# Performance work log

Measured on AMD Instinct MI355X. Metric: run time of the kernel, lower is better.

## Reference

```python
import jax, jax.numpy as jnp
import numpy as np

N, E, IN_DIM, OUT_DIM, EDGE_DIM = 50000, 800000, 256, 128, 64
NEG_SLOPE = 0.2


def setup_inputs() -> dict:
    key = jax.random.key(0)
    ks = jax.random.split(key, 8)
    xavier = lambda k, shape: jax.random.normal(k, shape, jnp.float32) * np.float32(np.sqrt(2.0 / (shape[0] + shape[1])))
    return {
        "nfeat": jax.random.normal(ks[0], (N, IN_DIM), jnp.float32),
        "ex": jax.random.normal(ks[1], (E, EDGE_DIM), jnp.float32),
        "src": jax.random.randint(ks[2], (E,), 0, N),
        "dst": jax.random.randint(ks[3], (E,), 0, N),
        "W_fc": xavier(ks[4], (OUT_DIM, IN_DIM)),
        "b_fc": jnp.zeros((OUT_DIM,), jnp.float32),
        "W_att": xavier(ks[5], (1, 2 * OUT_DIM + EDGE_DIM)),
        "b_att": jnp.zeros((1,), jnp.float32),
        "W_edge": xavier(ks[6], (OUT_DIM, EDGE_DIM)),
        "b_edge": jnp.zeros((OUT_DIM,), jnp.float32),
        "W_eatt": xavier(ks[7], (EDGE_DIM, EDGE_DIM)),
        "b_eatt": jnp.zeros((EDGE_DIM,), jnp.float32),
    }


def reference(nfeat, ex, src, dst, W_fc, b_fc, W_att, b_att, W_edge, b_edge, W_eatt, b_eatt):
    n = nfeat.shape[0]
    # node transform: z = fc(nfeat)  [N, OUT]
    z = nfeat @ W_fc.T + b_fc
    # edge transform for attention score calc  [E, EDGE_DIM]
    ex_t = ex @ W_eatt.T + b_eatt
    z_src = z[src]                                   # [E, OUT] gather
    # attention logits on concat[z_src, z_dst, ex_t]  [E, 1]
    z2 = jnp.concatenate([z_src, z[dst], ex_t], axis=1)
    e = jax.nn.leaky_relu(z2 @ W_att.T + b_att, NEG_SLOPE)
    # edge feature message  [E, OUT]
    ez = ex @ W_edge.T + b_edge
    # segment softmax over incoming edges of each dst node
    m = jax.ops.segment_max(e, dst, num_segments=n)  # [N, 1]
    w = jnp.exp(e - m[dst])
    denom = jax.ops.segment_sum(w, dst, num_segments=n)
    alpha = w / denom[dst]                           # [E, 1]
    # h = sum_e alpha * z_src + sum_e alpha * ez (apply_attention_on_edge)
    h = jax.ops.segment_sum(alpha * (z_src + ez), dst, num_segments=n)  # [N, OUT]
    return h, alpha
```

## Files before the change

### kernel.cpp

```cpp
#include <hip/hip_runtime.h>
#include <math.h>
#include <float.h>

#define IN_D 256
#define OUT_D 128
#define ED_D 64
#define NEG 0.2f

typedef __attribute__((ext_vector_type(8))) short bf16x8;
typedef __attribute__((ext_vector_type(4))) float f32x4;

__device__ __forceinline__ unsigned short f2bf(float f) {
    unsigned u = __float_as_uint(f);
    unsigned r = (u + 0x7FFFu + ((u >> 16) & 1u)) >> 16;
    return (unsigned short)r;
}
__device__ __forceinline__ float bf2f(unsigned short h) {
    return __uint_as_float((unsigned)h << 16);
}

__global__ __launch_bounds__(256) void k_init(
        const float* __restrict__ W_att, const float* __restrict__ b_att,
        const float* __restrict__ W_eatt, const float* __restrict__ b_eatt,
        const float* __restrict__ W_fc, const float* __restrict__ W_edge,
        float* __restrict__ u, float* __restrict__ c0,
        unsigned short* __restrict__ Wb, float2* __restrict__ Wt2,
        int* __restrict__ cnt, int N) {
    int idx = blockIdx.x * 256 + threadIdx.x;
    if (idx < N) cnt[idx] = 0;
    if (idx < IN_D * OUT_D) {
        int i = idx & 7;
        int lane = (idx >> 3) & 63;
        int rest = idx >> 9;
        int nt = rest & 7, ks = rest >> 3;
        int col = nt * 16 + (lane & 15);
        int k = ks * 32 + (lane >> 4) * 8 + i;
        Wb[idx] = f2bf(W_fc[col * IN_D + k]);
    }
    if (idx < ED_D * (OUT_D / 2)) {
        int k = idx >> 6, l = idx & 63;
        Wt2[idx] = make_float2(W_edge[(2 * l) * ED_D + k], W_edge[(2 * l + 1) * ED_D + k]);
    }
    if (idx < ED_D) {
        float acc = 0.f;
        for (int j = 0; j < ED_D; ++j) acc += W_att[256 + j] * W_eatt[j * ED_D + idx];
        u[idx] = acc;
    }
    if (idx == ED_D) {
        float c = 0.f;
        for (int j = 0; j < ED_D; ++j) c += W_att[256 + j] * b_eatt[j];
        c0[0] = c + b_att[0];
    }
}

__global__ __launch_bounds__(256) void k_hist(const int* __restrict__ dst,
                                              int* __restrict__ cnt,
                                              int* __restrict__ rank, int E) {
    int i = blockIdx.x * 256 + threadIdx.x;
    if (i < E) rank[i] = atomicAdd(&cnt[dst[i]], 1);
}

#define LDA 272
__global__ __launch_bounds__(256) void k_node(
        const float* __restrict__ nfeat, const unsigned short* __restrict__ Wb,
        const float* __restrict__ b_fc, const float* __restrict__ W_att,
        unsigned short* __restrict__ zb, float* __restrict__ asrc,
        float* __restrict__ adst, int n) {
    __shared__ unsigned short sa[128 * LDA];
    int t = threadIdx.x;
    int row_base = blockIdx.x * 128;

    int r8 = t >> 3, c8 = t & 7;
#pragma unroll
    for (int p = 0; p < 4; ++p) {
        int r = p * 32 + r8;
        int node = row_base + r; if (node >= n) node = n - 1;
        const float4* srcp = (const float4*)(nfeat + (size_t)node * IN_D);
#pragma unroll
        for (int q = 0; q < 8; ++q) {
            int c4 = q * 8 + c8;
            float4 v = srcp[c4];
            unsigned pk0 = (unsigned)f2bf(v.x) | ((unsigned)f2bf(v.y) << 16);
            unsigned pk1 = (unsigned)f2bf(v.z) | ((unsigned)f2bf(v.w) << 16);
            *(uint2*)&sa[(size_t)r * LDA + c4 * 4] = make_uint2(pk0, pk1);
        }
    }
    __syncthreads();

    int lane = t & 63, w = t >> 6;
    int lr = lane & 15, lg = lane >> 4;

    f32x4 acc[2][8];
#pragma unroll
    for (int mi = 0; mi < 2; ++mi)
#pragma unroll
        for (int nt = 0; nt < 8; ++nt) acc[mi][nt] = (f32x4)(0.f);

    const bf16x8* wb8 = (const bf16x8*)Wb;
#pragma unroll
    for (int ks = 0; ks < 8; ++ks) {
        bf16x8 af[2], bfr[8];
#pragma unroll
        for (int mi = 0; mi < 2; ++mi) {
            int row = (2 * w + mi) * 16 + lr;
            af[mi] = *(const bf16x8*)&sa[(size_t)row * LDA + ks * 32 + lg * 8];
        }
#pragma unroll
        for (int nt = 0; nt < 8; ++nt)
            bfr[nt] = wb8[(ks * 8 + nt) * 64 + lane];
#pragma unroll
        for (int mi = 0; mi < 2; ++mi)
#pragma unroll
            for (int nt = 0; nt < 8; ++nt)
                acc[mi][nt] = __builtin_amdgcn_mfma_f32_16x16x32_bf16(
                    af[mi], bfr[nt], acc[mi][nt], 0, 0, 0);
    }

    float w1c[8], w2c[8], bfc[8];
#pragma unroll
    for (int nt = 0; nt < 8; ++nt) {
        int col = nt * 16 + lr;
        w1c[nt] = W_att[col];
        w2c[nt] = W_att[128 + col];
        bfc[nt] = b_fc[col];
    }
#pragma unroll
    for (int mi = 0; mi < 2; ++mi) {
        float p1[4] = {0.f, 0.f, 0.f, 0.f}, p2[4] = {0.f, 0.f, 0.f, 0.f};
#pragma unroll
        for (int nt = 0; nt < 8; ++nt) {
#pragma unroll
            for (int reg = 0; reg < 4; ++reg) {
                float zv = acc[mi][nt][reg] + bfc[nt];
                int m = row_base + (2 * w + mi) * 16 + lg * 4 + reg;
                if (m < n) zb[(size_t)m * OUT_D + nt * 16 + lr] = f2bf(zv);
                p1[reg] = fmaf(zv, w1c[nt], p1[reg]);
                p2[reg] = fmaf(zv, w2c[nt], p2[reg]);
            }
        }
#pragma unroll
        for (int reg = 0; reg < 4; ++reg) {
#pragma unroll
            for (int off = 1; off <= 8; off <<= 1) {
                p1[reg] += __shfl_xor(p1[reg], off);
                p2[reg] += __shfl_xor(p2[reg], off);
            }
        }
        if (lr == 0) {
#pragma unroll
            for (int reg = 0; reg < 4; ++reg) {
                int m = row_base + (2 * w + mi) * 16 + lg * 4 + reg;
                if (m < n) { asrc[m] = p1[reg]; adst[m] = p2[reg]; }
            }
        }
    }
}

__global__ __launch_bounds__(1024) void k_scan(const int* __restrict__ cnt,
                                               int* __restrict__ rowptr, int N) {
    int t = threadIdx.x;
    int per = (N + 1023) / 1024;
    int b0 = t * per, b1 = b0 + per;
    if (b0 > N) b0 = N;
    if (b1 > N) b1 = N;
    int s = 0;
    for (int i = b0; i < b1; ++i) s += cnt[i];
    int wl = t & 63, w = t >> 6;
    int v = s;
#pragma unroll
    for (int off = 1; off < 64; off <<= 1) {
        int a = __shfl_up(v, off);
        if (wl >= off) v += a;
    }
    __shared__ int wsum[16], woff[16];
    if (wl == 63) wsum[w] = v;
    __syncthreads();
    if (t == 0) { int r = 0; for (int i = 0; i < 16; ++i) { woff[i] = r; r += wsum[i]; } }
    __syncthreads();
    int run = woff[w] + v - s;
    for (int i = b0; i < b1; ++i) { rowptr[i] = run; run += cnt[i]; }
    if (t == 1023) rowptr[N] = run;
}

__global__ __launch_bounds__(256) void k_fill(
        const int* __restrict__ dst, const int* __restrict__ src,
        const int* __restrict__ rank, const int* __restrict__ rowptr,
        int* __restrict__ eid_csr, int* __restrict__ src_csr, int E) {
    int i = blockIdx.x * 256 + threadIdx.x;
    if (i >= E) return;
    int d = dst[i];
    int pos = rowptr[d] + rank[i];
    eid_csr[pos] = i;
    src_csr[pos] = src[i];
}

__global__ __launch_bounds__(256) void k_fused(
        const unsigned short* __restrict__ zb, const float* __restrict__ ex,
        const int* __restrict__ eid_csr, const int* __restrict__ src_csr,
        const int* __restrict__ rowptr,
        const float* __restrict__ asrc, const float* __restrict__ adst,
        const float* __restrict__ u, const float* __restrict__ c0,
        float* __restrict__ h, float* __restrict__ alpha_out,
        float* __restrict__ xsum, int N) {
    int lane = threadIdx.x & 63;
    int half = lane >> 5, hl = lane & 31;
    int n = blockIdx.x * 4 + (threadIdx.x >> 6);
    if (n >= N) return;
    int beg = rowptr[n], end = rowptr[n + 1];
    int deg = end - beg;
    if (deg == 0) return;
    float adn = adst[n], cc = c0[0];
    const float2* ex2 = (const float2*)ex;
    const ushort4* z4 = (const ushort4*)zb;

    if (deg <= 64) {
        int el = 0, sl = 0;
        if (lane < deg) {
            el = eid_csr[beg + lane];
            sl = src_csr[beg + lane];
        }
        int qh = lane >> 4, ql = lane & 15;
        const float4* ex4 = (const float4*)ex;
        float4 u4q = ((const float4*)u)[ql];
        float lg = -FLT_MAX;
        for (int j = 0; j < deg; j += 4) {
            int jq = j + qh;
            int eq = __shfl(el, (jq < deg) ? jq : (deg - 1));
            float4 xv = ex4[(size_t)eq * 16 + ql];
            float d = fmaf(xv.x, u4q.x, fmaf(xv.y, u4q.y, fmaf(xv.z, u4q.z, xv.w * u4q.w)));
            d += __shfl_xor(d, 8);
            d += __shfl_xor(d, 4);
            d += __shfl_xor(d, 2);
            d += __shfl_xor(d, 1);
            int rel = lane - j;
            float dl = __shfl(d, (rel & 3) * 16);
            if (rel >= 0 && rel < 4 && lane < deg) lg = dl;
        }
        if (lane < deg) {
            lg += asrc[sl] + adn + cc;
            lg = (lg > 0.f) ? lg : NEG * lg;
        }
        float m = lg;
#pragma unroll
        for (int off = 32; off >= 1; off >>= 1) m = fmaxf(m, __shfl_xor(m, off));
        float wvv = (lane < deg) ? expf(lg - m) : 0.f;
        float sw = wvv;
#pragma unroll
        for (int off = 32; off >= 1; off >>= 1) sw += __shfl_xor(sw, off);
        float al = wvv / sw;
        if (lane < deg) alpha_out[el] = al;
        float4 accz = make_float4(0.f, 0.f, 0.f, 0.f);
        float2 accx = make_float2(0.f, 0.f);
        int j = 0;
        for (; j + 8 <= deg; j += 8) {
            float a[4]; int s[4], e[4];
#pragma unroll
            for (int q = 0; q < 4; ++q) {
                int idx = j + 2 * q + half;
                a[q] = __shfl(al, idx);
                s[q] = __shfl(sl, idx);
                e[q] = __shfl(el, idx);
            }
            ushort4 zu[4]; float2 xv[4];
#pragma unroll
            for (int q = 0; q < 4; ++q) {
                zu[q] = z4[(size_t)s[q] * 32 + hl];
                xv[q] = ex2[(size_t)e[q] * 32 + hl];
            }
#pragma unroll
            for (int q = 0; q < 4; ++q) {
                accz.x = fmaf(a[q], bf2f(zu[q].x), accz.x);
                accz.y = fmaf(a[q], bf2f(zu[q].y), accz.y);
                accz.z = fmaf(a[q], bf2f(zu[q].z), accz.z);
                accz.w = fmaf(a[q], bf2f(zu[q].w), accz.w);
                accx.x = fmaf(a[q], xv[q].x, accx.x);
                accx.y = fmaf(a[q], xv[q].y, accx.y);
            }
        }
        if (j + 4 <= deg) {
            float a[2]; int s[2], e[2];
#pragma unroll
            for (int q = 0; q < 2; ++q) {
                int idx = j + 2 * q + half;
                a[q] = __shfl(al, idx);
                s[q] = __shfl(sl, idx);
                e[q] = __shfl(el, idx);
            }
            ushort4 zu[2]; float2 xv[2];
#pragma unroll
            for (int q = 0; q < 2; ++q) {
                zu[q] = z4[(size_t)s[q] * 32 + hl];
                xv[q] = ex2[(size_t)e[q] * 32 + hl];
            }
#pragma unroll
            for (int q = 0; q < 2; ++q) {
                accz.x = fmaf(a[q], bf2f(zu[q].x), accz.x);
                accz.y = fmaf(a[q], bf2f(zu[q].y), accz.y);
                accz.z = fmaf(a[q], bf2f(zu[q].z), accz.z);
                accz.w = fmaf(a[q], bf2f(zu[q].w), accz.w);
                accx.x = fmaf(a[q], xv[q].x, accx.x);
                accx.y = fmaf(a[q], xv[q].y, accx.y);
            }
            j += 4;
        }
        for (; j < deg; j += 2) {
            int idx = j + half;
            float a = __shfl(al, idx);
            int s = __shfl(sl, idx), e = __shfl(el, idx);
            ushort4 zu = z4[(size_t)s * 32 + hl];
            float2 xv = ex2[(size_t)e * 32 + hl];
            accz.x = fmaf(a, bf2f(zu.x), accz.x);
            accz.y = fmaf(a, bf2f(zu.y), accz.y);
            accz.z = fmaf(a, bf2f(zu.z), accz.z);
            accz.w = fmaf(a, bf2f(zu.w), accz.w);
            accx.x = fmaf(a, xv.x, accx.x);
            accx.y = fmaf(a, xv.y, accx.y);
        }
        accz.x += __shfl_xor(accz.x, 32);
        accz.y += __shfl_xor(accz.y, 32);
        accz.z += __shfl_xor(accz.z, 32);
        accz.w += __shfl_xor(accz.w, 32);
        accx.x += __shfl_xor(accx.x, 32);
        accx.y += __shfl_xor(accx.y, 32);
        if (half == 0) {
            ((float4*)h)[(size_t)n * 32 + hl] = accz;
            ((float2*)xsum)[(size_t)n * 32 + hl] = accx;
        }
    } else {
        float uv = u[lane];
        float m = -FLT_MAX, ssum = 0.f;
        for (int i = beg; i < end; ++i) {
            int e = eid_csr[i];
            float xv = ex[(size_t)e * ED_D + lane];
            float p = xv * uv;
#pragma unroll
            for (int off = 32; off >= 1; off >>= 1) p += __shfl_xor(p, off);
            float lg = p + asrc[src_csr[i]] + adn + cc;
            lg = (lg > 0.f) ? lg : NEG * lg;
            float mn = fmaxf(m, lg);
            ssum = ssum * expf(m - mn) + expf(lg - mn);
            m = mn;
        }
        float rden = 1.f / ssum;
        const ushort2* z2 = (const ushort2*)zb;
        float2 accz2 = make_float2(0.f, 0.f);
        float accxs = 0.f;
        for (int i = beg; i < end; ++i) {
            int e = eid_csr[i];
            int s = src_csr[i];
            float xv = ex[(size_t)e * ED_D + lane];
            float p = xv * uv;
#pragma unroll
            for (int off = 32; off >= 1; off >>= 1) p += __shfl_xor(p, off);
            float lg = p + asrc[s] + adn + cc;
            lg = (lg > 0.f) ? lg : NEG * lg;
            float al = expf(lg - m) * rden;
            if (lane == 0) alpha_out[e] = al;
            accxs = fmaf(al, xv, accxs);
            ushort2 zz = z2[(size_t)s * ED_D + lane];
            accz2.x = fmaf(al, bf2f(zz.x), accz2.x);
            accz2.y = fmaf(al, bf2f(zz.y), accz2.y);
        }
        ((float2*)h)[(size_t)n * ED_D + lane] = accz2;
        xsum[(size_t)n * ED_D + lane] = accxs;
    }
}

__global__ __launch_bounds__(256) void k_xmm(
        const float2* __restrict__ Wt2, const float* __restrict__ b_edge,
        const float* __restrict__ xsum, const int* __restrict__ rowptr,
        float2* __restrict__ h2, int N) {
    __shared__ float2 swt[ED_D * 64];
    for (int i = threadIdx.x; i < ED_D * 64; i += 256) swt[i] = Wt2[i];
    __syncthreads();
    int lane = threadIdx.x & 63;
    int wv = threadIdx.x >> 6;
    float2 be2 = ((const float2*)b_edge)[lane];
    for (int n = blockIdx.x * 4 + wv; n < N; n += gridDim.x * 4) {
        int deg = rowptr[n + 1] - rowptr[n];
        if (deg == 0) {
            h2[(size_t)n * 64 + lane] = make_float2(0.f, 0.f);
            continue;
        }
        float xk = xsum[(size_t)n * 64 + lane];
        float2 hv = h2[(size_t)n * 64 + lane];
        hv.x += be2.x; hv.y += be2.y;
#pragma unroll 8
        for (int k = 0; k < 64; ++k) {
            float a = __shfl(xk, k);
            float2 w2 = swt[k * 64 + lane];
            hv.x = fmaf(a, w2.x, hv.x);
            hv.y = fmaf(a, w2.y, hv.y);
        }
        h2[(size_t)n * 64 + lane] = hv;
    }
}

extern "C" void kernel_launch(void* const* d_in, const int* in_sizes, int n_in,
                              void* d_out, int out_size, void* d_ws, size_t ws_size,
                              hipStream_t stream) {
    const float* nfeat = (const float*)d_in[0];
    const float* ex    = (const float*)d_in[1];
    const int*   src   = (const int*)d_in[2];
    const int*   dst   = (const int*)d_in[3];
    const float* W_fc  = (const float*)d_in[4];
    const float* b_fc  = (const float*)d_in[5];
    const float* W_att = (const float*)d_in[6];
    const float* b_att = (const float*)d_in[7];
    const float* W_edge = (const float*)d_in[8];
    const float* b_edge = (const float*)d_in[9];
    const float* W_eatt = (const float*)d_in[10];
    const float* b_eatt = (const float*)d_in[11];
    int N = in_sizes[0] / IN_D;
    int E = in_sizes[2];

    float* h_out = (float*)d_out;
    float* alpha_out = h_out + (size_t)N * OUT_D;

    char* w = (char*)d_ws;
    auto alloc = [&](size_t bytes) { char* p = w; w += (bytes + 255) & ~255ull; return p; };
    unsigned short* zb = (unsigned short*)alloc((size_t)N * OUT_D * 2);
    float* asrc   = (float*)alloc((size_t)N * 4);
    float* adst   = (float*)alloc((size_t)N * 4);
    int* cnt      = (int*)alloc((size_t)N * 4);
    int* rowptr   = (int*)alloc(((size_t)N + 1) * 4);
    int* rank     = (int*)alloc((size_t)E * 4);
    int* eid_csr  = (int*)alloc((size_t)E * 4);
    int* src_csr  = (int*)alloc((size_t)E * 4);
    float* xsum   = (float*)alloc((size_t)N * ED_D * 4);
    unsigned short* Wb = (unsigned short*)alloc((size_t)IN_D * OUT_D * 2);
    float2* Wt2   = (float2*)alloc((size_t)ED_D * 64 * 8);
    float* u      = (float*)alloc(64 * 4);
    float* c0     = (float*)alloc(4);

    int init_total = N > IN_D * OUT_D ? N : IN_D * OUT_D;
    k_init<<<(init_total + 255) / 256, 256, 0, stream>>>(
        W_att, b_att, W_eatt, b_eatt, W_fc, W_edge, u, c0, Wb, Wt2, cnt, N);
    k_hist<<<(E + 255) / 256, 256, 0, stream>>>(dst, cnt, rank, E);
    k_node<<<(N + 127) / 128, 256, 0, stream>>>(nfeat, Wb, b_fc, W_att, zb, asrc, adst, N);
    k_scan<<<1, 1024, 0, stream>>>(cnt, rowptr, N);
    k_fill<<<(E + 255) / 256, 256, 0, stream>>>(dst, src, rank, rowptr, eid_csr, src_csr, E);
    k_fused<<<(N + 3) / 4, 256, 0, stream>>>(zb, ex, eid_csr, src_csr, rowptr, asrc, adst,
                                             u, c0, h_out, alpha_out, xsum, N);
    k_xmm<<<(N + 3) / 4, 256, 0, stream>>>((const float2*)Wt2, b_edge, xsum, rowptr,
                                           (float2*)h_out, N);
}
```

Measured before the change: 349.0 us.

## Assign one half-wave per destination node and pack CSR indices as int2

The fused aggregation kernel now assigns 32 lanes per destination node, eight nodes per block, instead of a full 64-lane wavefront per node. Average degree is about 16, so the wider mapping left many lanes idle. The cross-half reduction is gone, and the high-degree path now uses vectorised float2/ushort4 loads over 32 lanes. Edge id and source id are also packed into one int2 CSR array, so each edge needs one load instead of two. The risks are serialised gathers per edge within a half-wave and a lower degree threshold for the slower online-softmax path.

Result: slower. 380.9 us (+9.1%).

```diff
diff --git a/kernel.cpp b/kernel.cpp
--- a/kernel.cpp
+++ b/kernel.cpp
@@ -185,81 +185,81 @@
 __global__ __launch_bounds__(256) void k_fill(
         const int* __restrict__ dst, const int* __restrict__ src,
         const int* __restrict__ rank, const int* __restrict__ rowptr,
-        int* __restrict__ eid_csr, int* __restrict__ src_csr, int E) {
+        int2* __restrict__ csr2, int E) {
     int i = blockIdx.x * 256 + threadIdx.x;
     if (i >= E) return;
     int d = dst[i];
     int pos = rowptr[d] + rank[i];
-    eid_csr[pos] = i;
-    src_csr[pos] = src[i];
+    csr2[pos] = make_int2(i, src[i]);
 }
 
 __global__ __launch_bounds__(256) void k_fused(
         const unsigned short* __restrict__ zb, const float* __restrict__ ex,
-        const int* __restrict__ eid_csr, const int* __restrict__ src_csr,
-        const int* __restrict__ rowptr,
+        const int2* __restrict__ csr2, const int* __restrict__ rowptr,
         const float* __restrict__ asrc, const float* __restrict__ adst,
         const float* __restrict__ u, const float* __restrict__ c0,
         float* __restrict__ h, float* __restrict__ alpha_out,
         float* __restrict__ xsum, int N) {
-    int lane = threadIdx.x & 63;
-    int half = lane >> 5, hl = lane & 31;
-    int n = blockIdx.x * 4 + (threadIdx.x >> 6);
+    int hl = threadIdx.x & 31;
+    int hb = (threadIdx.x & 63) & 32;
+    int n = blockIdx.x * 8 + (threadIdx.x >> 5);
     if (n >= N) return;
     int beg = rowptr[n], end = rowptr[n + 1];
     int deg = end - beg;
     if (deg == 0) return;
     float adn = adst[n], cc = c0[0];
     const float2* ex2 = (const float2*)ex;
+    const float4* ex4 = (const float4*)ex;
     const ushort4* z4 = (const ushort4*)zb;
 
-    if (deg <= 64) {
+    if (deg <= 32) {
         int el = 0, sl = 0;
-        if (lane < deg) {
-            el = eid_csr[beg + lane];
-            sl = src_csr[beg + lane];
-        }
-        int qh = lane >> 4, ql = lane & 15;
-        const float4* ex4 = (const float4*)ex;
+        if (hl < deg) { int2 r = csr2[beg + hl]; el = r.x; sl = r.y; }
+        int qq = hl >> 4, ql = hl & 15;
         float4 u4q = ((const float4*)u)[ql];
         float lg = -FLT_MAX;
-        for (int j = 0; j < deg; j += 4) {
-            int jq = j + qh;
-            int eq = __shfl(el, (jq < deg) ? jq : (deg - 1));
+        for (int j = 0; j < deg; j += 2) {
+            int jq = j + qq;
+            int eq = __shfl(el, hb + ((jq < deg) ? jq : (deg - 1)));
             float4 xv = ex4[(size_t)eq * 16 + ql];
             float d = fmaf(xv.x, u4q.x, fmaf(xv.y, u4q.y, fmaf(xv.z, u4q.z, xv.w * u4q.w)));
             d += __shfl_xor(d, 8);
             d += __shfl_xor(d, 4);
             d += __shfl_xor(d, 2);
             d += __shfl_xor(d, 1);
-            int rel = lane - j;
-            float dl = __shfl(d, (rel & 3) * 16);
-            if (rel >= 0 && rel < 4 && lane < deg) lg = dl;
-        }
-        if (lane < deg) {
+            int rel = hl - j;
+            float dl = __shfl(d, hb + (rel & 1) * 16);
+            if (rel >= 0 && rel < 2 && hl < deg) lg = dl;
+        }
+        if (hl < deg) {
             lg += asrc[sl] + adn + cc;
             lg = (lg > 0.f) ? lg : NEG * lg;
         }
         float m = lg;
-#pragma unroll
-        for (int off = 32; off >= 1; off >>= 1) m = fmaxf(m, __shfl_xor(m, off));
-        float wvv = (lane < deg) ? expf(lg - m) : 0.f;
+        m = fmaxf(m, __shfl_xor(m, 16));
+        m = fmaxf(m, __shfl_xor(m, 8));
+        m = fmaxf(m, __shfl_xor(m, 4));
+        m = fmaxf(m, __shfl_xor(m, 2));
+        m = fmaxf(m, __shfl_xor(m, 1));
+        float wvv = (hl < deg) ? expf(lg - m) : 0.f;
         float sw = wvv;
-#pragma unroll
-        for (int off = 32; off >= 1; off >>= 1) sw += __shfl_xor(sw, off);
+        sw += __shfl_xor(sw, 16);
+        sw += __shfl_xor(sw, 8);
+        sw += __shfl_xor(sw, 4);
+        sw += __shfl_xor(sw, 2);
+        sw += __shfl_xor(sw, 1);
         float al = wvv / sw;
-        if (lane < deg) alpha_out[el] = al;
+        if (hl < deg) alpha_out[el] = al;
         float4 accz = make_float4(0.f, 0.f, 0.f, 0.f);
         float2 accx = make_float2(0.f, 0.f);
         int j = 0;
-        for (; j + 8 <= deg; j += 8) {
+        for (; j + 4 <= deg; j += 4) {
             float a[4]; int s[4], e[4];
 #pragma unroll
             for (int q = 0; q < 4; ++q) {
-                int idx = j + 2 * q + half;
-                a[q] = __shfl(al, idx);
-                s[q] = __shfl(sl, idx);
-                e[q] = __shfl(el, idx);
+                a[q] = __shfl(al, hb + j + q);
+                s[q] = __shfl(sl, hb + j + q);
+                e[q] = __shfl(el, hb + j + q);
             }
             ushort4 zu[4]; float2 xv[4];
 #pragma unroll
@@ -277,36 +277,9 @@
                 accx.y = fmaf(a[q], xv[q].y, accx.y);
             }
         }
-        if (j + 4 <= deg) {
-            float a[2]; int s[2], e[2];
-#pragma unroll
-            for (int q = 0; q < 2; ++q) {
-                int idx = j + 2 * q + half;
-                a[q] = __shfl(al, idx);
-                s[q] = __shfl(sl, idx);
-                e[q] = __shfl(el, idx);
-            }
-            ushort4 zu[2]; float2 xv[2];
-#pragma unroll
-            for (int q = 0; q < 2; ++q) {
-                zu[q] = z4[(size_t)s[q] * 32 + hl];
-                xv[q] = ex2[(size_t)e[q] * 32 + hl];
-            }
-#pragma unroll
-            for (int q = 0; q < 2; ++q) {
-                accz.x = fmaf(a[q], bf2f(zu[q].x), accz.x);
-                accz.y = fmaf(a[q], bf2f(zu[q].y), accz.y);
-                accz.z = fmaf(a[q], bf2f(zu[q].z), accz.z);
-                accz.w = fmaf(a[q], bf2f(zu[q].w), accz.w);
-                accx.x = fmaf(a[q], xv[q].x, accx.x);
-                accx.y = fmaf(a[q], xv[q].y, accx.y);
-            }
-            j += 4;
-        }
-        for (; j < deg; j += 2) {
-            int idx = j + half;
-            float a = __shfl(al, idx);
-            int s = __shfl(sl, idx), e = __shfl(el, idx);
+        for (; j < deg; ++j) {
+            float a = __shfl(al, hb + j);
+            int s = __shfl(sl, hb + j), e = __shfl(el, hb + j);
             ushort4 zu = z4[(size_t)s * 32 + hl];
             float2 xv = ex2[(size_t)e * 32 + hl];
             accz.x = fmaf(a, bf2f(zu.x), accz.x);
@@ -316,53 +289,52 @@
             accx.x = fmaf(a, xv.x, accx.x);
             accx.y = fmaf(a, xv.y, accx.y);
         }
-        accz.x += __shfl_xor(accz.x, 32);
-        accz.y += __shfl_xor(accz.y, 32);
-        accz.z += __shfl_xor(accz.z, 32);
-        accz.w += __shfl_xor(accz.w, 32);
-        accx.x += __shfl_xor(accx.x, 32);
-        accx.y += __shfl_xor(accx.y, 32);
-        if (half == 0) {
-            ((float4*)h)[(size_t)n * 32 + hl] = accz;
-            ((float2*)xsum)[(size_t)n * 32 + hl] = accx;
-        }
+        ((float4*)h)[(size_t)n * 32 + hl] = accz;
+        ((float2*)xsum)[(size_t)n * 32 + hl] = accx;
     } else {
-        float uv = u[lane];
+        float2 u2 = ((const float2*)u)[hl];
         float m = -FLT_MAX, ssum = 0.f;
         for (int i = beg; i < end; ++i) {
-            int e = eid_csr[i];
-            float xv = ex[(size_t)e * ED_D + lane];
-            float p = xv * uv;
-#pragma unroll
-            for (int off = 32; off >= 1; off >>= 1) p += __shfl_xor(p, off);
-            float lg = p + asrc[src_csr[i]] + adn + cc;
-            lg = (lg > 0.f) ? lg : NEG * lg;
-            float mn = fmaxf(m, lg);
-            ssum = ssum * expf(m - mn) + expf(lg - mn);
+            int2 r = csr2[i];
+            float2 xv = ex2[(size_t)r.x * 32 + hl];
+            float p = fmaf(xv.x, u2.x, xv.y * u2.y);
+            p += __shfl_xor(p, 16);
+            p += __shfl_xor(p, 8);
+            p += __shfl_xor(p, 4);
+            p += __shfl_xor(p, 2);
+            p += __shfl_xor(p, 1);
+            float lgv = p + asrc[r.y] + adn + cc;
+            lgv = (lgv > 0.f) ? lgv : NEG * lgv;
+            float mn = fmaxf(m, lgv);
+            ssum = ssum * expf(m - mn) + expf(lgv - mn);
             m = mn;
         }
         float rden = 1.f / ssum;
-        const ushort2* z2 = (const ushort2*)zb;
-        float2 accz2 = make_float2(0.f, 0.f);
-        float accxs = 0.f;
+        float4 accz = make_float4(0.f, 0.f, 0.f, 0.f);
+        float2 accx = make_float2(0.f, 0.f);
         for (int i = beg; i < end; ++i) {
-            int e = eid_csr[i];
-            int s = src_csr[i];
-            float xv = ex[(size_t)e * ED_D + lane];
-            float p = xv * uv;
-#pragma unroll
-            for (int off = 32; off >= 1; off >>= 1) p += __shfl_xor(p, off);
-            float lg = p + asrc[s] + adn + cc;
-            lg = (lg > 0.f) ? lg : NEG * lg;
-            float al = expf(lg - m) * rden;
-            if (lane == 0) alpha_out[e] = al;
-            accxs = fmaf(al, xv, accxs);
-            ushort2 zz = z2[(size_t)s * ED_D + lane];
-            accz2.x = fmaf(al, bf2f(zz.x), accz2.x);
-            accz2.y = fmaf(al, bf2f(zz.y), accz2.y);
-        }
-        ((float2*)h)[(size_t)n * ED_D + lane] = accz2;
-        xsum[(size_t)n * ED_D + lane] = accxs;
+            int2 r = csr2[i];
+            float2 xv = ex2[(size_t)r.x * 32 + hl];
+            float p = fmaf(xv.x, u2.x, xv.y * u2.y);
+            p += __shfl_xor(p, 16);
+            p += __shfl_xor(p, 8);
+            p += __shfl_xor(p, 4);
+            p += __shfl_xor(p, 2);
+            p += __shfl_xor(p, 1);
+            float lgv = p + asrc[r.y] + adn + cc;
+            lgv = (lgv > 0.f) ? lgv : NEG * lgv;
+            float al = expf(lgv - m) * rden;
+            if (hl == 0) alpha_out[r.x] = al;
+            ushort4 zu = z4[(size_t)r.y * 32 + hl];
+            accz.x = fmaf(al, bf2f(zu.x), accz.x);
+            accz.y = fmaf(al, bf2f(zu.y), accz.y);
+            accz.z = fmaf(al, bf2f(zu.z), accz.z);
+            accz.w = fmaf(al, bf2f(zu.w), accz.w);
+            accx.x = fmaf(al, xv.x, accx.x);
+            accx.y = fmaf(al, xv.y, accx.y);
+        }
+        ((float4*)h)[(size_t)n * 32 + hl] = accz;
+        ((float2*)xsum)[(size_t)n * 32 + hl] = accx;
     }
 }
 
@@ -425,8 +397,7 @@
     int* cnt      = (int*)alloc((size_t)N * 4);
     int* rowptr   = (int*)alloc(((size_t)N + 1) * 4);
     int* rank     = (int*)alloc((size_t)E * 4);
-    int* eid_csr  = (int*)alloc((size_t)E * 4);
-    int* src_csr  = (int*)alloc((size_t)E * 4);
+    int2* csr2    = (int2*)alloc((size_t)E * 8);
     float* xsum   = (float*)alloc((size_t)N * ED_D * 4);
     unsigned short* Wb = (unsigned short*)alloc((size_t)IN_D * OUT_D * 2);
     float2* Wt2   = (float2*)alloc((size_t)ED_D * 64 * 8);
@@ -439,8 +410,8 @@
     k_hist<<<(E + 255) / 256, 256, 0, stream>>>(dst, cnt, rank, E);
     k_node<<<(N + 127) / 128, 256, 0, stream>>>(nfeat, Wb, b_fc, W_att, zb, asrc, adst, N);
     k_scan<<<1, 1024, 0, stream>>>(cnt, rowptr, N);
-    k_fill<<<(E + 255) / 256, 256, 0, stream>>>(dst, src, rank, rowptr, eid_csr, src_csr, E);
-    k_fused<<<(N + 3) / 4, 256, 0, stream>>>(zb, ex, eid_csr, src_csr, rowptr, asrc, adst,
+    k_fill<<<(E + 255) / 256, 256, 0, stream>>>(dst, src, rank, rowptr, csr2, E);
+    k_fused<<<(N + 7) / 8, 256, 0, stream>>>(zb, ex, csr2, rowptr, asrc, adst,
                                              u, c0, h_out, alpha_out, xsum, N);
     k_xmm<<<(N + 3) / 4, 256, 0, stream>>>((const float2*)Wt2, b_edge, xsum, rowptr,
                                            (float2*)h_out, N);
```
